# Kernel tuning notes

Measured on AMD Instinct MI355X. Metric: run time of the kernel, lower is better.

## Reference

```python
import jax, jax.numpy as jnp
import numpy as np

EPS = 1e-5


def clin(xr, xi, Wr, Wi, br, bi):
    # complex linear layer: (xr + i xi) @ (Wr + i Wi) + (br + i bi)
    yr = xr @ Wr - xi @ Wi + br
    yi = xr @ Wi + xi @ Wr + bi
    return yr, yi


def setup_inputs() -> dict:
    key = jax.random.key(0)
    ks = jax.random.split(key, 16)
    B, N, DE, DV = 4, 256, 128, 64
    s_in = 1.0 / np.sqrt(DE)
    s_p = 1.0 / np.sqrt(DV)
    f32 = jnp.float32
    inp = {
        'Z_q': jax.random.normal(ks[0], (B, 2, N, DE), f32),
        'Z_k': jax.random.normal(ks[1], (B, 2, N, DE), f32),
        'Z_v': jax.random.normal(ks[2], (B, 2, N, DE), f32),
        't_measure_all': jnp.tile(jnp.arange(N + 1, dtype=f32) * 0.01, (B, 1)),
        'Wq_r': jax.random.normal(ks[3], (DE, DV), f32) * s_in,
        'Wq_i': jax.random.normal(ks[4], (DE, DV), f32) * s_in,
        'bq_r': jnp.zeros((DV,), f32), 'bq_i': jnp.zeros((DV,), f32),
        'Wk_r': jax.random.normal(ks[5], (DE, DV), f32) * s_in,
        'Wk_i': jax.random.normal(ks[6], (DE, DV), f32) * s_in,
        'bk_r': jnp.zeros((DV,), f32), 'bk_i': jnp.zeros((DV,), f32),
        'Wv_r': jax.random.normal(ks[7], (DE, DV), f32) * s_in,
        'Wv_i': jax.random.normal(ks[8], (DE, DV), f32) * s_in,
        'bv_r': jnp.zeros((DV,), f32), 'bv_i': jnp.zeros((DV,), f32),
        'Wp_r': jax.random.normal(ks[9], (DV, DE), f32) * s_p,
        'Wp_i': jax.random.normal(ks[10], (DV, DE), f32) * s_p,
        'bp_r': jnp.zeros((DE,), f32), 'bp_i': jnp.zeros((DE,), f32),
        'lambda1': jax.random.normal(ks[11], (2, DV // 2), f32),
        'lambda_Omega_sqrt': jax.random.normal(ks[12], (DV,), f32) / DV,
        'lambda_Gamma_sqrt': jax.random.normal(ks[13], (DV,), f32) / DV,
        'noise_floor': jnp.array(1.0, f32),
        'tau': jnp.array(1.0, f32),
        'nu': jnp.array(1.0, f32),
        'eta_param': jnp.zeros((DV,), f32),
    }
    return inp


def reference(Z_q, Z_k, Z_v, t_measure_all,
              Wq_r, Wq_i, bq_r, bq_i, Wk_r, Wk_i, bk_r, bk_i,
              Wv_r, Wv_i, bv_r, bv_i, Wp_r, Wp_i, bp_r, bp_i,
              lambda1, lambda_Omega_sqrt, lambda_Gamma_sqrt,
              noise_floor, tau, nu, eta_param):
    N = Z_q.shape[2]
    # complex projections (B, N, d)
    Qr, Qi = clin(Z_q[:, 0], Z_q[:, 1], Wq_r, Wq_i, bq_r, bq_i)
    Kr_, Ki_ = clin(Z_k[:, 0], Z_k[:, 1], Wk_r, Wk_i, bk_r, bk_i)
    Vr, Vi = clin(Z_v[:, 0], Z_v[:, 1], Wv_r, Wv_i, bv_r, bv_i)
    # state-transition eigenvalues: stable conjugate pairs
    re = jnp.concatenate([-lambda1[0] ** 2, -lambda1[0] ** 2])  # (d_v,), Re<=0
    im = jnp.concatenate([lambda1[1], -lambda1[1]])             # (d_v,)
    lam_Om = lambda_Omega_sqrt ** 2
    lam_Ga = lambda_Gamma_sqrt ** 2 + EPS
    # pairwise complex exponential kernel exp(lambda * (t_i - t_j))
    t = t_measure_all[0, :-1]                       # (N,)
    dt = t[:, None] - t[None, :]                    # (N, N)
    amp = jnp.exp(re[None, None, :] * dt[:, :, None])
    ph = im[None, None, :] * dt[:, :, None]
    Ker = amp * jnp.cos(ph)                          # (N, N, d_v)
    Kei = amp * jnp.sin(ph)
    # propagated value estimates Z_hat_ij = exp(lam dt_ij) * V_j
    Zhr = Ker[None] * Vr[:, None] - Kei[None] * Vi[:, None]  # (B, N, N, d_v)
    Zhi = Ker[None] * Vi[:, None] + Kei[None] * Vr[:, None]
    # residuals R_ij = Q_i - exp(lam dt_ij) * K_j
    Rr = Qr[:, :, None, :] - (Ker[None] * Kr_[:, None] - Kei[None] * Ki_[:, None])
    Ri = Qi[:, :, None, :] - (Ker[None] * Ki_[:, None] + Kei[None] * Kr_[:, None])
    # per-pair covariance (OU-process propagation of measurement + process noise)
    adt = jnp.abs(dt)[:, :, None]
    exp2 = jnp.exp(2.0 * re * adt)                   # (N, N, d_v)
    Vij = lam_Ga * exp2 + lam_Om * (exp2 - 1.0) / (2.0 * (re - EPS))
    # mahalanobis distance and attention scores
    mah = (Rr ** 2 + Ri ** 2) / (Vij[None] + lam_Ga)          # (B, N, N, d_v)
    dist_sum = jnp.abs(nu) * jnp.sum(mah, axis=3, keepdims=True)
    base = Vij[None] * (noise_floor + dist_sum + EPS)
    scores = -jnp.abs(tau) * jnp.log(base)
    mask = jnp.tril(jnp.ones((N, N), bool))
    scores = jnp.where(mask[None, :, :, None], scores, -jnp.inf)
    Qij = jax.nn.softmax(scores, axis=2)             # normalize over j
    m = mask[None, :, :, None].astype(Zhr.dtype)
    Zhr = Zhr * m
    Zhi = Zhi * m
    est_vr = jnp.einsum('bijd,bijd->bid', Qij, Zhr)
    est_vi = jnp.einsum('bijd,bijd->bid', Qij, Zhi)
    # gated residual mix (double sigmoid as in source)
    eta = jax.nn.sigmoid(eta_param)
    g = jax.nn.sigmoid(eta)
    elr = (1.0 - eta) * Vr + g * est_vr
    eli = (1.0 - eta) * Vi + g * est_vi
    # one-step-ahead prediction via matrix exponential exp(lambda * h)
    h = t[1] - t[0]
    ma = jnp.exp(re * h)
    mr, mi = ma * jnp.cos(im * h), ma * jnp.sin(im * h)
    ppr = mr * elr - mi * eli
    ppi = mr * eli + mi * elr
    outr, outi = clin(ppr, ppi, Wp_r, Wp_i, bp_r, bp_i)
    est_latent = jnp.stack([elr, eli], axis=1)       # (B, 2, N, d_v)
    out = jnp.stack([outr, outi], axis=1)            # (B, 2, N, d_e)
    Zhat = jnp.stack([Zhr, Zhi], axis=1)             # (B, 2, N, N, d_v)
    lambda_h = jnp.stack([re, im])                   # (2, d_v)
    return est_latent, out, Qij, Zhat, lambda_h
```

## Files before the change

### kernel.cpp

```cpp
#include <hip/hip_runtime.h>
#include <math.h>

#define B_ 4
#define N_ 256
#define DE_ 128
#define DV_ 64
#define EPS_ 1e-5f

typedef __attribute__((ext_vector_type(4))) float f32x4;

__device__ __forceinline__ f32x4 ld4(const float* p) { return *(const f32x4*)p; }
__device__ __forceinline__ void st4(float* p, f32x4 v) { *(f32x4*)p = v; }
__device__ __forceinline__ void nt4(float* p, f32x4 v) { __builtin_nontemporal_store(v, (f32x4*)p); }
__device__ __forceinline__ f32x4 exp4(f32x4 a) {
    f32x4 r; r[0]=expf(a[0]); r[1]=expf(a[1]); r[2]=expf(a[2]); r[3]=expf(a[3]); return r;
}
__device__ __forceinline__ f32x4 max4(f32x4 a, f32x4 b) {
    f32x4 r; r[0]=fmaxf(a[0],b[0]); r[1]=fmaxf(a[1],b[1]); r[2]=fmaxf(a[2],b[2]); r[3]=fmaxf(a[3],b[3]); return r;
}

#define OFF_ETA   0
#define OFF_G     64
#define OFF_MR    128
#define OFF_MI    192
#define OFF_KER   256
#define OFF_KEI   (OFF_KER + N_*DV_)
#define OFF_LOGV  (OFF_KEI + N_*DV_)
#define OFF_INV   (OFF_LOGV + N_*DV_)
#define OFF_QR    (OFF_INV + N_*DV_)
#define OFF_QI    (OFF_QR + B_*N_*DV_)
#define OFF_KR    (OFF_QI + B_*N_*DV_)
#define OFF_KI    (OFF_KR + B_*N_*DV_)
#define OFF_VR    (OFF_KI + B_*N_*DV_)
#define OFF_VI    (OFF_VR + B_*N_*DV_)

#define OUT_EL    0
#define OUT_OUT   (B_*2*N_*DV_)
#define OUT_QIJ   (OUT_OUT + B_*2*N_*DE_)
#define OUT_ZHAT  (OUT_QIJ + B_*N_*N_*DV_)
#define OUT_LAMH  (OUT_ZHAT + (size_t)B_*2*N_*N_*DV_)

__global__ __launch_bounds__(256) void k_pre(
    const float* __restrict__ Zq, const float* __restrict__ Zk, const float* __restrict__ Zv,
    const float* __restrict__ Wqr, const float* __restrict__ Wqi,
    const float* __restrict__ bqr, const float* __restrict__ bqi,
    const float* __restrict__ Wkr, const float* __restrict__ Wki,
    const float* __restrict__ bkr, const float* __restrict__ bki,
    const float* __restrict__ Wvr, const float* __restrict__ Wvi,
    const float* __restrict__ bvr, const float* __restrict__ bvi,
    const float* __restrict__ t,  const float* __restrict__ lam1,
    const float* __restrict__ lOm, const float* __restrict__ lGa,
    const float* __restrict__ eta_p,
    float* __restrict__ ws, float* __restrict__ out)
{
    const int tid = (int)threadIdx.x;

    if (blockIdx.x >= 1024) {
        const int idx = (int)blockIdx.x - 1024;
        const int w = tid >> 6;
        const int d = tid & 63;
        const int delta = idx * 4 + w;

        const float l0 = lam1[d & 31];
        const float re = -l0 * l0;
        const float im = (d < 32) ? lam1[32 + d] : -lam1[d];

        const float lo = lOm[d];
        const float lam_Om = lo * lo;
        const float lg_ = lGa[d];
        const float lam_Ga = lg_ * lg_ + EPS_;

        const float t0 = t[0];
        const float dt = t[delta] - t0;

        const float amp = expf(re * dt);
        const float ph  = im * dt;
        const int td = delta * DV_ + d;
        ws[OFF_KER + td] = amp * cosf(ph);
        ws[OFF_KEI + td] = amp * sinf(ph);

        const float e2  = expf(2.0f * re * dt);
        const float vij = lam_Ga * e2 + lam_Om * (e2 - 1.0f) / (2.0f * (re - EPS_));
        ws[OFF_LOGV + td] = logf(vij);
        ws[OFF_INV  + td] = 1.0f / (vij + lam_Ga);

        if (delta == 0) {
            const float eta = 1.0f / (1.0f + expf(-eta_p[d]));
            const float g   = 1.0f / (1.0f + expf(-eta));
            ws[OFF_ETA + d] = eta;
            ws[OFF_G   + d] = g;
            const float h  = t[1] - t0;
            const float ma = expf(re * h);
            ws[OFF_MR + d] = ma * cosf(im * h);
            ws[OFF_MI + d] = ma * sinf(im * h);
            out[OUT_LAMH + d]       = re;
            out[OUT_LAMH + DV_ + d] = im;
        }
        return;
    }

    const int row = (int)blockIdx.x;
    const int b = row >> 8, n = row & (N_ - 1);

    __shared__ float x[6][DE_];
    __shared__ float red[4][6][DV_];

    if (tid < DE_) {
        x[0][tid] = Zq[((size_t)(b*2+0)*N_ + n)*DE_ + tid];
        x[1][tid] = Zq[((size_t)(b*2+1)*N_ + n)*DE_ + tid];
        x[2][tid] = Zk[((size_t)(b*2+0)*N_ + n)*DE_ + tid];
        x[3][tid] = Zk[((size_t)(b*2+1)*N_ + n)*DE_ + tid];
        x[4][tid] = Zv[((size_t)(b*2+0)*N_ + n)*DE_ + tid];
        x[5][tid] = Zv[((size_t)(b*2+1)*N_ + n)*DE_ + tid];
    }
    __syncthreads();

    const int w = tid >> 6;
    const int d = tid & 63;
    float aqr = 0.f, aqi = 0.f, akr = 0.f, aki = 0.f, avr = 0.f, avi = 0.f;
    const int k0 = w * 32;
    #pragma unroll 4
    for (int kk = 0; kk < 32; ++kk) {
        const int k = k0 + kk;
        const float xqr = x[0][k], xqi = x[1][k];
        const float xkr = x[2][k], xki = x[3][k];
        const float xvr = x[4][k], xvi = x[5][k];
        float wr, wi;
        wr = Wqr[k*DV_ + d]; wi = Wqi[k*DV_ + d];
        aqr += xqr*wr - xqi*wi; aqi += xqr*wi + xqi*wr;
        wr = Wkr[k*DV_ + d]; wi = Wki[k*DV_ + d];
        akr += xkr*wr - xki*wi; aki += xkr*wi + xki*wr;
        wr = Wvr[k*DV_ + d]; wi = Wvi[k*DV_ + d];
        avr += xvr*wr - xvi*wi; avi += xvr*wi + xvi*wr;
    }
    red[w][0][d] = aqr; red[w][1][d] = aqi;
    red[w][2][d] = akr; red[w][3][d] = aki;
    red[w][4][d] = avr; red[w][5][d] = avi;
    __syncthreads();

    if (tid < DV_) {
        const int o = row * DV_ + tid;
        ws[OFF_QR + o] = red[0][0][tid]+red[1][0][tid]+red[2][0][tid]+red[3][0][tid] + bqr[tid];
        ws[OFF_QI + o] = red[0][1][tid]+red[1][1][tid]+red[2][1][tid]+red[3][1][tid] + bqi[tid];
        ws[OFF_KR + o] = red[0][2][tid]+red[1][2][tid]+red[2][2][tid]+red[3][2][tid] + bkr[tid];
        ws[OFF_KI + o] = red[0][3][tid]+red[1][3][tid]+red[2][3][tid]+red[3][3][tid] + bki[tid];
        ws[OFF_VR + o] = red[0][4][tid]+red[1][4][tid]+red[2][4][tid]+red[3][4][tid] + bvr[tid];
        ws[OFF_VI + o] = red[0][5][tid]+red[1][5][tid]+red[2][5][tid]+red[3][5][tid] + bvi[tid];
    }
}

__global__ __launch_bounds__(256) void k_main2(
    const float* __restrict__ ws, float* __restrict__ out,
    const float* __restrict__ Wpr, const float* __restrict__ Wpi,
    const float* __restrict__ bpr, const float* __restrict__ bpi,
    const float* __restrict__ nf_p, const float* __restrict__ tau_p,
    const float* __restrict__ nu_p)
{
    const int row = (int)blockIdx.x;
    const int b = row >> 8, i = row & (N_ - 1);
    const int tid = (int)threadIdx.x;
    const int w = tid >> 6;
    const int l = tid & 63;
    const int g = l >> 4;
    const int q16 = l & 15;
    const int dq = q16 * 4;

    __shared__ float lb[N_];
    __shared__ f32x4 redM[4][16];
    __shared__ f32x4 redS[4][16];
    __shared__ f32x4 redR[4][16];
    __shared__ f32x4 redI[4][16];
    __shared__ float ppr_s[DV_], ppi_s[DV_];

    const float nf    = nf_p[0];
    const float tau_a = fabsf(tau_p[0]);
    const float nu_a  = fabsf(nu_p[0]);

    const f32x4 qr4 = ld4(ws + OFF_QR + row*DV_ + dq);
    const f32x4 qi4 = ld4(ws + OFF_QI + row*DV_ + dq);

    f32x4 m4 = {-3.0e38f, -3.0e38f, -3.0e38f, -3.0e38f};
    f32x4 s4 = {0.f, 0.f, 0.f, 0.f};
    for (int jb = 4*w; jb <= i; jb += 16) {
        const int j = jb + g;
        const bool act = (j <= i);
        const int delta = act ? (i - j) : 0;
        const int td = delta*DV_ + dq;
        const f32x4 ker = ld4(ws + OFF_KER  + td);
        const f32x4 kei = ld4(ws + OFF_KEI  + td);
        const f32x4 vnv = ld4(ws + OFF_INV  + td);
        const f32x4 lgv = ld4(ws + OFF_LOGV + td);
        const int kj = (b*N_ + (act ? j : 0))*DV_ + dq;
        const f32x4 kr = ld4(ws + OFF_KR + kj);
        const f32x4 ki = ld4(ws + OFF_KI + kj);
        const f32x4 rr = qr4 - (ker*kr - kei*ki);
        const f32x4 ri = qi4 - (ker*ki + kei*kr);
        const f32x4 mah = (rr*rr + ri*ri) * vnv;
        float ds = mah[0] + mah[1] + mah[2] + mah[3];
        ds += __shfl_xor(ds, 1);
        ds += __shfl_xor(ds, 2);
        ds += __shfl_xor(ds, 4);
        ds += __shfl_xor(ds, 8);
        const float lg = logf(nf + nu_a*ds + EPS_);
        if (act) {
            if (q16 == 0) lb[j] = lg;
            const f32x4 sc = (-tau_a) * (lgv + lg);
            const f32x4 mn = max4(m4, sc);
            s4 = s4 * exp4(m4 - mn) + exp4(sc - mn);
            m4 = mn;
        }
    }
    #pragma unroll
    for (int mask = 16; mask <= 32; mask <<= 1) {
        f32x4 mo, so;
        #pragma unroll
        for (int c = 0; c < 4; ++c) { mo[c] = __shfl_xor(m4[c], mask); so[c] = __shfl_xor(s4[c], mask); }
        const f32x4 mn = max4(m4, mo);
        s4 = s4 * exp4(m4 - mn) + so * exp4(mo - mn);
        m4 = mn;
    }
    if (g == 0) { redM[w][q16] = m4; redS[w][q16] = s4; }
    __syncthreads();
    f32x4 M = redM[0][q16], S = redS[0][q16];
    #pragma unroll
    for (int w2 = 1; w2 < 4; ++w2) {
        const f32x4 mo = redM[w2][q16], so = redS[w2][q16];
        const f32x4 mn = max4(M, mo);
        S = S * exp4(M - mn) + so * exp4(mo - mn);
        M = mn;
    }
    const f32x4 one = {1.f, 1.f, 1.f, 1.f};
    const f32x4 inv = one / S;

    f32x4 evr = {0.f,0.f,0.f,0.f}, evi = {0.f,0.f,0.f,0.f};
    float* qij  = out + OUT_QIJ + (size_t)row * N_ * DV_;
    float* zro  = out + OUT_ZHAT + ((size_t)(b*2+0)*N_ + i) * N_ * DV_;
    float* zio  = out + OUT_ZHAT + ((size_t)(b*2+1)*N_ + i) * N_ * DV_;
    const f32x4 z4 = {0.f,0.f,0.f,0.f};
    for (int jb = 4*w; jb < N_; jb += 16) {
        const int j = jb + g;
        const int o = j*DV_ + dq;
        if (j <= i) {
            const int td = (i - j)*DV_ + dq;
            const f32x4 lgv = ld4(ws + OFF_LOGV + td);
            const f32x4 ker = ld4(ws + OFF_KER + td);
            const f32x4 kei = ld4(ws + OFF_KEI + td);
            const float lg = lb[j];
            const f32x4 q4 = exp4((-tau_a)*(lgv + lg) - M) * inv;
            nt4(qij + o, q4);
            const int vj = (b*N_ + j)*DV_ + dq;
            const f32x4 vr = ld4(ws + OFF_VR + vj);
            const f32x4 vi = ld4(ws + OFF_VI + vj);
            const f32x4 zr = ker*vr - kei*vi;
            const f32x4 zi = ker*vi + kei*vr;
            nt4(zro + o, zr);
            nt4(zio + o, zi);
            evr += q4 * zr;
            evi += q4 * zi;
        } else {
            nt4(qij + o, z4);
            nt4(zro + o, z4);
            nt4(zio + o, z4);
        }
    }
    #pragma unroll
    for (int mask = 16; mask <= 32; mask <<= 1) {
        #pragma unroll
        for (int c = 0; c < 4; ++c) {
            evr[c] += __shfl_xor(evr[c], mask);
            evi[c] += __shfl_xor(evi[c], mask);
        }
    }
    if (g == 0) { redR[w][q16] = evr; redI[w][q16] = evi; }
    __syncthreads();

    if (tid < 16) {
        const f32x4 Evr = redR[0][tid] + redR[1][tid] + redR[2][tid] + redR[3][tid];
        const f32x4 Evi = redI[0][tid] + redI[1][tid] + redI[2][tid] + redI[3][tid];
        const int dq2 = tid * 4;
        const f32x4 vr  = ld4(ws + OFF_VR + row*DV_ + dq2);
        const f32x4 vi  = ld4(ws + OFF_VI + row*DV_ + dq2);
        const f32x4 eta = ld4(ws + OFF_ETA + dq2);
        const f32x4 gg  = ld4(ws + OFF_G + dq2);
        const f32x4 elr = (1.0f - eta)*vr + gg*Evr;
        const f32x4 eli = (1.0f - eta)*vi + gg*Evi;
        st4(out + OUT_EL + ((size_t)(b*2+0)*N_ + i)*DV_ + dq2, elr);
        st4(out + OUT_EL + ((size_t)(b*2+1)*N_ + i)*DV_ + dq2, eli);
        const f32x4 mr = ld4(ws + OFF_MR + dq2);
        const f32x4 mi = ld4(ws + OFF_MI + dq2);
        st4(ppr_s + dq2, mr*elr - mi*eli);
        st4(ppi_s + dq2, mr*eli + mi*elr);
    }
    __syncthreads();

    if (tid < DE_) {
        const int e = tid;
        float ar = bpr[e], ai = bpi[e];
        #pragma unroll 8
        for (int dd = 0; dd < DV_; ++dd) {
            const float wr = Wpr[dd*DE_ + e], wi = Wpi[dd*DE_ + e];
            const float r = ppr_s[dd], im = ppi_s[dd];
            ar += r*wr - im*wi;
            ai += r*wi + im*wr;
        }
        out[OUT_OUT + ((size_t)(b*2+0)*N_ + i)*DE_ + e] = ar;
        out[OUT_OUT + ((size_t)(b*2+1)*N_ + i)*DE_ + e] = ai;
    }
}

extern "C" void kernel_launch(void* const* d_in, const int* in_sizes, int n_in,
                              void* d_out, int out_size, void* d_ws, size_t ws_size,
                              hipStream_t stream)
{
    const float* Zq   = (const float*)d_in[0];
    const float* Zk   = (const float*)d_in[1];
    const float* Zv   = (const float*)d_in[2];
    const float* t    = (const float*)d_in[3];
    const float* Wqr  = (const float*)d_in[4];
    const float* Wqi  = (const float*)d_in[5];
    const float* bqr  = (const float*)d_in[6];
    const float* bqi  = (const float*)d_in[7];
    const float* Wkr  = (const float*)d_in[8];
    const float* Wki  = (const float*)d_in[9];
    const float* bkr  = (const float*)d_in[10];
    const float* bki  = (const float*)d_in[11];
    const float* Wvr  = (const float*)d_in[12];
    const float* Wvi  = (const float*)d_in[13];
    const float* bvr  = (const float*)d_in[14];
    const float* bvi  = (const float*)d_in[15];
    const float* Wpr  = (const float*)d_in[16];
    const float* Wpi  = (const float*)d_in[17];
    const float* bpr  = (const float*)d_in[18];
    const float* bpi  = (const float*)d_in[19];
    const float* lam1 = (const float*)d_in[20];
    const float* lOm  = (const float*)d_in[21];
    const float* lGa  = (const float*)d_in[22];
    const float* nf   = (const float*)d_in[23];
    const float* tau  = (const float*)d_in[24];
    const float* nu   = (const float*)d_in[25];
    const float* etap = (const float*)d_in[26];

    float* ws  = (float*)d_ws;
    float* out = (float*)d_out;

    k_pre<<<1024 + 64, 256, 0, stream>>>(Zq, Zk, Zv,
                                         Wqr, Wqi, bqr, bqi,
                                         Wkr, Wki, bkr, bki,
                                         Wvr, Wvi, bvr, bvi,
                                         t, lam1, lOm, lGa, etap, ws, out);
    k_main2<<<B_*N_, 256, 0, stream>>>(ws, out, Wpr, Wpi, bpr, bpi, nf, tau, nu);
}
```

Baseline: 72.94 us.

## Process four rows per projection block, fold softmax normalizer, use regular stores

The projection kernel now handles four rows per block, one wave per row, with vectorized loads of the inputs into shared memory. Each wave runs the full K loop itself, which removes the cross-wave shared reduction and cuts the grid from 1024 to 256 projection blocks while reusing weight loads across rows through cache. In the main kernel the softmax normalization is folded into the exponent by subtracting log(S) instead of multiplying by 1/S. The nontemporal stores for the large Qij and Zhat outputs are replaced by ordinary stores, which may change cache behaviour for this write-heavy output.

Result: slower. 83.60 us (+14.6%).

```diff
diff --git a/kernel.cpp b/kernel.cpp
--- a/kernel.cpp
+++ b/kernel.cpp
@@ -11,12 +11,14 @@
 
 __device__ __forceinline__ f32x4 ld4(const float* p) { return *(const f32x4*)p; }
 __device__ __forceinline__ void st4(float* p, f32x4 v) { *(f32x4*)p = v; }
-__device__ __forceinline__ void nt4(float* p, f32x4 v) { __builtin_nontemporal_store(v, (f32x4*)p); }
 __device__ __forceinline__ f32x4 exp4(f32x4 a) {
     f32x4 r; r[0]=expf(a[0]); r[1]=expf(a[1]); r[2]=expf(a[2]); r[3]=expf(a[3]); return r;
 }
 __device__ __forceinline__ f32x4 max4(f32x4 a, f32x4 b) {
     f32x4 r; r[0]=fmaxf(a[0],b[0]); r[1]=fmaxf(a[1],b[1]); r[2]=fmaxf(a[2],b[2]); r[3]=fmaxf(a[3],b[3]); return r;
+}
+__device__ __forceinline__ f32x4 log4(f32x4 a) {
+    f32x4 r; r[0]=logf(a[0]); r[1]=logf(a[1]); r[2]=logf(a[2]); r[3]=logf(a[3]); return r;
 }
 
 #define OFF_ETA   0
@@ -54,11 +56,11 @@
     float* __restrict__ ws, float* __restrict__ out)
 {
     const int tid = (int)threadIdx.x;
-
-    if (blockIdx.x >= 1024) {
-        const int idx = (int)blockIdx.x - 1024;
-        const int w = tid >> 6;
-        const int d = tid & 63;
+    const int w = tid >> 6;
+    const int d = tid & 63;
+
+    if (blockIdx.x >= 256) {
+        const int idx = (int)blockIdx.x - 256;
         const int delta = idx * 4 + w;
 
         const float l0 = lam1[d & 31];
@@ -99,32 +101,33 @@
         return;
     }
 
-    const int row = (int)blockIdx.x;
-    const int b = row >> 8, n = row & (N_ - 1);
-
-    __shared__ float x[6][DE_];
-    __shared__ float red[4][6][DV_];
-
-    if (tid < DE_) {
-        x[0][tid] = Zq[((size_t)(b*2+0)*N_ + n)*DE_ + tid];
-        x[1][tid] = Zq[((size_t)(b*2+1)*N_ + n)*DE_ + tid];
-        x[2][tid] = Zk[((size_t)(b*2+0)*N_ + n)*DE_ + tid];
-        x[3][tid] = Zk[((size_t)(b*2+1)*N_ + n)*DE_ + tid];
-        x[4][tid] = Zv[((size_t)(b*2+0)*N_ + n)*DE_ + tid];
-        x[5][tid] = Zv[((size_t)(b*2+1)*N_ + n)*DE_ + tid];
+    const int row0 = (int)blockIdx.x * 4;
+    const int b = row0 >> 8;
+    const int n0 = row0 & (N_ - 1);
+
+    __shared__ float x[4][6][DE_];
+    #pragma unroll
+    for (int it = 0; it < 3; ++it) {
+        const int v = tid + it * 256;
+        const int seg = v >> 5;
+        const int pos = v & 31;
+        const int r = seg & 3;
+        const int a = seg >> 2;
+        const int m = a >> 1;
+        const int c = a & 1;
+        const float* src = (m == 0) ? Zq : ((m == 1) ? Zk : Zv);
+        const f32x4 val = ld4(src + ((size_t)(b*2 + c)*N_ + (n0 + r))*DE_ + pos*4);
+        st4(&x[r][a][pos*4], val);
     }
     __syncthreads();
 
-    const int w = tid >> 6;
-    const int d = tid & 63;
+    const int row = row0 + w;
     float aqr = 0.f, aqi = 0.f, akr = 0.f, aki = 0.f, avr = 0.f, avi = 0.f;
-    const int k0 = w * 32;
-    #pragma unroll 4
-    for (int kk = 0; kk < 32; ++kk) {
-        const int k = k0 + kk;
-        const float xqr = x[0][k], xqi = x[1][k];
-        const float xkr = x[2][k], xki = x[3][k];
-        const float xvr = x[4][k], xvi = x[5][k];
+    #pragma unroll 8
+    for (int k = 0; k < DE_; ++k) {
+        const float xqr = x[w][0][k], xqi = x[w][1][k];
+        const float xkr = x[w][2][k], xki = x[w][3][k];
+        const float xvr = x[w][4][k], xvi = x[w][5][k];
         float wr, wi;
         wr = Wqr[k*DV_ + d]; wi = Wqi[k*DV_ + d];
         aqr += xqr*wr - xqi*wi; aqi += xqr*wi + xqi*wr;
@@ -133,20 +136,13 @@
         wr = Wvr[k*DV_ + d]; wi = Wvi[k*DV_ + d];
         avr += xvr*wr - xvi*wi; avi += xvr*wi + xvi*wr;
     }
-    red[w][0][d] = aqr; red[w][1][d] = aqi;
-    red[w][2][d] = akr; red[w][3][d] = aki;
-    red[w][4][d] = avr; red[w][5][d] = avi;
-    __syncthreads();
-
-    if (tid < DV_) {
-        const int o = row * DV_ + tid;
-        ws[OFF_QR + o] = red[0][0][tid]+red[1][0][tid]+red[2][0][tid]+red[3][0][tid] + bqr[tid];
-        ws[OFF_QI + o] = red[0][1][tid]+red[1][1][tid]+red[2][1][tid]+red[3][1][tid] + bqi[tid];
-        ws[OFF_KR + o] = red[0][2][tid]+red[1][2][tid]+red[2][2][tid]+red[3][2][tid] + bkr[tid];
-        ws[OFF_KI + o] = red[0][3][tid]+red[1][3][tid]+red[2][3][tid]+red[3][3][tid] + bki[tid];
-        ws[OFF_VR + o] = red[0][4][tid]+red[1][4][tid]+red[2][4][tid]+red[3][4][tid] + bvr[tid];
-        ws[OFF_VI + o] = red[0][5][tid]+red[1][5][tid]+red[2][5][tid]+red[3][5][tid] + bvi[tid];
-    }
+    const int o = row * DV_ + d;
+    ws[OFF_QR + o] = aqr + bqr[d];
+    ws[OFF_QI + o] = aqi + bqi[d];
+    ws[OFF_KR + o] = akr + bkr[d];
+    ws[OFF_KI + o] = aki + bki[d];
+    ws[OFF_VR + o] = avr + bvr[d];
+    ws[OFF_VI + o] = avi + bvi[d];
 }
 
 __global__ __launch_bounds__(256) void k_main2(
@@ -229,8 +225,7 @@
         S = S * exp4(M - mn) + so * exp4(mo - mn);
         M = mn;
     }
-    const f32x4 one = {1.f, 1.f, 1.f, 1.f};
-    const f32x4 inv = one / S;
+    const f32x4 C = M + log4(S);
 
     f32x4 evr = {0.f,0.f,0.f,0.f}, evi = {0.f,0.f,0.f,0.f};
     float* qij  = out + OUT_QIJ + (size_t)row * N_ * DV_;
@@ -246,21 +241,21 @@
             const f32x4 ker = ld4(ws + OFF_KER + td);
             const f32x4 kei = ld4(ws + OFF_KEI + td);
             const float lg = lb[j];
-            const f32x4 q4 = exp4((-tau_a)*(lgv + lg) - M) * inv;
-            nt4(qij + o, q4);
+            const f32x4 q4 = exp4((-tau_a)*(lgv + lg) - C);
+            st4(qij + o, q4);
             const int vj = (b*N_ + j)*DV_ + dq;
             const f32x4 vr = ld4(ws + OFF_VR + vj);
             const f32x4 vi = ld4(ws + OFF_VI + vj);
             const f32x4 zr = ker*vr - kei*vi;
             const f32x4 zi = ker*vi + kei*vr;
-            nt4(zro + o, zr);
-            nt4(zio + o, zi);
+            st4(zro + o, zr);
+            st4(zio + o, zi);
             evr += q4 * zr;
             evi += q4 * zi;
         } else {
-            nt4(qij + o, z4);
-            nt4(zro + o, z4);
-            nt4(zio + o, z4);
+            st4(qij + o, z4);
+            st4(zro + o, z4);
+            st4(zio + o, z4);
         }
     }
     #pragma unroll
@@ -343,10 +338,10 @@
     float* ws  = (float*)d_ws;
     float* out = (float*)d_out;
 
-    k_pre<<<1024 + 64, 256, 0, stream>>>(Zq, Zk, Zv,
-                                         Wqr, Wqi, bqr, bqi,
-                                         Wkr, Wki, bkr, bki,
-                                         Wvr, Wvi, bvr, bvi,
-                                         t, lam1, lOm, lGa, etap, ws, out);
+    k_pre<<<256 + 64, 256, 0, stream>>>(Zq, Zk, Zv,
+                                        Wqr, Wqi, bqr, bqi,
+                                        Wkr, Wki, bkr, bki,
+                                        Wvr, Wvi, bvr, bvi,
+                                        t, lam1, lOm, lGa, etap, ws, out);
     k_main2<<<B_*N_, 256, 0, stream>>>(ws, out, Wpr, Wpi, bpr, bpi, nf, tau, nu);
 }
```
